# Kernel optimization log

Measured on AMD Instinct MI355X. Metric: run time of the kernel, lower is better.

The kernel has to match this reference:

```python
import jax, jax.numpy as jnp
from jax import lax
import numpy as np

IN_C, OUT_C, K, N_SPLIT = 256, 256, 3, 4
N_LEGO = int(OUT_C * 0.25)          # 64
BASIC_C = IN_C // N_SPLIT           # 64


def setup_inputs() -> dict:
    key = jax.random.key(0)
    k1, k2, k3, k4 = jax.random.split(key, 4)
    x = jax.random.normal(k1, (32, IN_C, 56, 56), dtype=jnp.float32)
    # kaiming-normal-ish initialization of parameters
    lego = jax.random.normal(k2, (N_LEGO, BASIC_C, K, 1), dtype=jnp.float32) * np.sqrt(2.0 / (BASIC_C * K))
    aux_coefficients = jax.random.normal(k3, (N_SPLIT, OUT_C, N_LEGO, 1, 1), dtype=jnp.float32) * np.sqrt(2.0 / N_LEGO)
    aux_combination = jax.random.normal(k4, (N_SPLIT, OUT_C, N_LEGO, 1, 1), dtype=jnp.float32) * np.sqrt(2.0 / N_LEGO)
    return {"x": x, "lego": lego, "aux_coefficients": aux_coefficients, "aux_combination": aux_combination}


def reference(x, lego, aux_coefficients, aux_combination):
    n_split, out_c, n_lego = aux_combination.shape[:3]
    bc = lego.shape[1]
    # one-hot selection: each (split, out_channel) picks exactly one lego feature
    idx = jnp.argmax(aux_combination[..., 0, 0], axis=2)              # (n_split, out_c)
    proxy = jax.nn.one_hot(idx, n_lego, dtype=x.dtype)                # (n_split, out_c, n_lego)
    W = aux_coefficients[..., 0, 0] * proxy                           # (n_split, out_c, n_lego)
    out = 0.0
    for i in range(n_split):
        xi = x[:, i * bc:(i + 1) * bc]                                # (B, bc, H, W)
        feat = lax.conv_general_dilated(
            xi, lego, window_strides=(3, 1), padding=((1, 1), (1, 1)),
            dimension_numbers=("NCHW", "OIHW", "NCHW"))               # (B, n_lego, Ho, Wo)
        out = out + jnp.einsum("bnhw,on->bohw", feat, W[i])
    return out
```

## Files before the change

kernel.cpp:

```cpp
#include <hip/hip_runtime.h>

#define INC    256
#define HIN    56
#define WIN    56
#define HOUT   19
#define WOUT   58
#define KTOT   768

typedef short frag8 __attribute__((ext_vector_type(8)));
typedef float f32x4 __attribute__((ext_vector_type(4)));

static __device__ __forceinline__ unsigned short f2bf(float f) {
    unsigned u = __float_as_uint(f);
    u += 0x7fffu + ((u >> 16) & 1u);
    return (unsigned short)(u >> 16);
}

__global__ __launch_bounds__(256) void prep_weff(
    const float* __restrict__ lego,
    const float* __restrict__ coefs,
    const float* __restrict__ comb,
    unsigned short* __restrict__ Asw)
{
    __shared__ int   idxS[4];
    __shared__ float cofS[4];
    const int t  = threadIdx.x;
    const int kx = blockIdx.x;
    const int o  = blockIdx.y;
    const int wv = t >> 6, l = t & 63;

    float v  = comb[(wv * 256 + o) * 64 + l];
    int   bi = l;
    #pragma unroll
    for (int off = 32; off >= 1; off >>= 1) {
        float ov = __shfl_xor(v, off, 64);
        int   oi = __shfl_xor(bi, off, 64);
        if (ov > v || (ov == v && oi < bi)) { v = ov; bi = oi; }
    }
    if (l == 0) {
        idxS[wv] = bi;
        cofS[wv] = coefs[(wv * 256 + o) * 64 + bi];
    }
    __syncthreads();

    const int k  = kx * 256 + t;
    const int kh = k >> 8, c = k & 255;
    const int i  = c >> 6, cl = c & 63;
    float w = cofS[i] * lego[idxS[i] * 192 + cl * 3 + kh];

    const int o_tile = o >> 4, m = o & 15;
    const int ks = k >> 5, kc = (k >> 3) & 3, j = k & 7;
    Asw[((((size_t)o_tile * 24 + ks) * 64) + kc * 16 + m) * 8 + j] = f2bf(w);
}

__global__ __launch_bounds__(256, 5) void conv_mfma(
    const float* __restrict__ x,
    const unsigned short* __restrict__ Asw,
    float* __restrict__ out)
{
    __shared__ unsigned short Xs[12 * 2 * 64 * 8];

    const int t  = threadIdx.x;
    const int wh = blockIdx.x;
    const int h  = blockIdx.y;
    const int b  = blockIdx.z;

    const int l  = t & 63;
    const int lo = l & 15;
    const int hi = l >> 4;
    const int wv = t >> 6;

    f32x4 acc[4][2];
    #pragma unroll
    for (int ot = 0; ot < 4; ++ot)
        #pragma unroll
        for (int nt = 0; nt < 2; ++nt)
            acc[ot][nt] = (f32x4){0.f, 0.f, 0.f, 0.f};

    const float* xb = x + (size_t)b * (INC * HIN * WIN);
    const int w     = t & 31;
    const int kg    = t >> 5;
    const int col   = wh * 32 - 1 + w;
    const bool colok = (unsigned)col < (unsigned)WIN;
    const int wtile = w >> 4;
    const int lbase = w & 15;
    const int rowbase = 3 * h - 1;

    const frag8* Af = (const frag8*)Asw + ((size_t)(wv * 4) * 24) * 64 + l;
    const frag8* Xf = (const frag8*)Xs + l;

    for (int c2 = 0; c2 < 2; ++c2) {
        #pragma unroll
        for (int q = 0; q < 6; ++q) {
            int p   = kg * 6 + q;
            int ksl = p >> 2, kc = p & 3;
            int kgl = c2 * 384 + ksl * 32 + kc * 8;
            int kh  = kgl >> 8, c0 = kgl & 255;
            int row = rowbase + kh;
            bool ok = colok && ((unsigned)row < (unsigned)HIN);
            const float* xp = xb + (size_t)c0 * (HIN * WIN) + row * WIN + col;
            union { frag8 f; unsigned short u[8]; } pk;
            #pragma unroll
            for (int j = 0; j < 8; ++j) {
                float v = ok ? xp[(size_t)j * (HIN * WIN)] : 0.f;
                pk.u[j] = f2bf(v);
            }
            *(frag8*)&Xs[(((ksl * 2 + wtile) * 64) + kc * 16 + lbase) * 8] = pk.f;
        }
        __syncthreads();

        const int ksb = c2 * 12;
        frag8 a[4], an[4], b0, b1, b0n, b1n;
        #pragma unroll
        for (int ot = 0; ot < 4; ++ot) a[ot] = Af[(ot * 24 + ksb) * 64];
        b0 = Xf[0];
        b1 = Xf[64];

        #pragma unroll
        for (int ks = 0; ks < 11; ++ks) {
            #pragma unroll
            for (int ot = 0; ot < 4; ++ot) an[ot] = Af[(ot * 24 + ksb + ks + 1) * 64];
            b0n = Xf[((ks + 1) * 2) * 64];
            b1n = Xf[((ks + 1) * 2 + 1) * 64];

            #pragma unroll
            for (int ot = 0; ot < 4; ++ot) {
                acc[ot][0] = __builtin_amdgcn_mfma_f32_16x16x32_bf16(a[ot], b0, acc[ot][0], 0, 0, 0);
                acc[ot][1] = __builtin_amdgcn_mfma_f32_16x16x32_bf16(a[ot], b1, acc[ot][1], 0, 0, 0);
            }
            #pragma unroll
            for (int ot = 0; ot < 4; ++ot) a[ot] = an[ot];
            b0 = b0n; b1 = b1n;
        }
        #pragma unroll
        for (int ot = 0; ot < 4; ++ot) {
            acc[ot][0] = __builtin_amdgcn_mfma_f32_16x16x32_bf16(a[ot], b0, acc[ot][0], 0, 0, 0);
            acc[ot][1] = __builtin_amdgcn_mfma_f32_16x16x32_bf16(a[ot], b1, acc[ot][1], 0, 0, 0);
        }
        __syncthreads();
    }

    const int wb = wh * 32;
    const int obase = wv * 64;
    #pragma unroll
    for (int ot = 0; ot < 4; ++ot) {
        #pragma unroll
        for (int nt = 0; nt < 2; ++nt) {
            int wcol = wb + nt * 16 + lo;
            if (wcol < WOUT) {
                #pragma unroll
                for (int r = 0; r < 4; ++r) {
                    int o = obase + ot * 16 + hi * 4 + r;
                    out[((size_t)(b * 256 + o) * HOUT + h) * WOUT + wcol] = acc[ot][nt][r];
                }
            }
        }
    }
}

extern "C" void kernel_launch(void* const* d_in, const int* in_sizes, int n_in,
                              void* d_out, int out_size, void* d_ws, size_t ws_size,
                              hipStream_t stream) {
    const float* x     = (const float*)d_in[0];
    const float* lego  = (const float*)d_in[1];
    const float* coefs = (const float*)d_in[2];
    const float* comb  = (const float*)d_in[3];
    float* out = (float*)d_out;

    unsigned short* Asw = (unsigned short*)d_ws;

    prep_weff<<<dim3(3, 256), 256, 0, stream>>>(lego, coefs, comb, Asw);
    conv_mfma<<<dim3(2, HOUT, 32), 256, 0, stream>>>(x, Asw, out);
}
```

Measured before the change: 194.2 us.

## Prefetch second K-half of input into registers during first-half MFMA loop

Unrolls the two-chunk K loop so that global loads for the second half of the input tile are issued into 48 registers before the first half's MFMA loop runs. After the first compute phase those values are converted to bf16 and stored to shared memory. The goal is to hide global load latency behind MFMA work. The 48 extra live floats raise register pressure and may reduce occupancy under the launch_bounds(256,5) target.

```diff
diff --git a/kernel.cpp b/kernel.cpp
--- a/kernel.cpp
+++ b/kernel.cpp
@@ -70,13 +70,6 @@
     const int hi = l >> 4;
     const int wv = t >> 6;
 
-    f32x4 acc[4][2];
-    #pragma unroll
-    for (int ot = 0; ot < 4; ++ot)
-        #pragma unroll
-        for (int nt = 0; nt < 2; ++nt)
-            acc[ot][nt] = (f32x4){0.f, 0.f, 0.f, 0.f};
-
     const float* xb = x + (size_t)b * (INC * HIN * WIN);
     const int w     = t & 31;
     const int kg    = t >> 5;
@@ -89,55 +82,105 @@
     const frag8* Af = (const frag8*)Asw + ((size_t)(wv * 4) * 24) * 64 + l;
     const frag8* Xf = (const frag8*)Xs + l;
 
-    for (int c2 = 0; c2 < 2; ++c2) {
-        #pragma unroll
-        for (int q = 0; q < 6; ++q) {
-            int p   = kg * 6 + q;
-            int ksl = p >> 2, kc = p & 3;
-            int kgl = c2 * 384 + ksl * 32 + kc * 8;
-            int kh  = kgl >> 8, c0 = kgl & 255;
-            int row = rowbase + kh;
-            bool ok = colok && ((unsigned)row < (unsigned)HIN);
-            const float* xp = xb + (size_t)c0 * (HIN * WIN) + row * WIN + col;
-            union { frag8 f; unsigned short u[8]; } pk;
-            #pragma unroll
-            for (int j = 0; j < 8; ++j) {
-                float v = ok ? xp[(size_t)j * (HIN * WIN)] : 0.f;
-                pk.u[j] = f2bf(v);
-            }
-            *(frag8*)&Xs[(((ksl * 2 + wtile) * 64) + kc * 16 + lbase) * 8] = pk.f;
-        }
-        __syncthreads();
-
-        const int ksb = c2 * 12;
-        frag8 a[4], an[4], b0, b1, b0n, b1n;
-        #pragma unroll
-        for (int ot = 0; ot < 4; ++ot) a[ot] = Af[(ot * 24 + ksb) * 64];
-        b0 = Xf[0];
-        b1 = Xf[64];
-
-        #pragma unroll
-        for (int ks = 0; ks < 11; ++ks) {
-            #pragma unroll
-            for (int ot = 0; ot < 4; ++ot) an[ot] = Af[(ot * 24 + ksb + ks + 1) * 64];
-            b0n = Xf[((ks + 1) * 2) * 64];
-            b1n = Xf[((ks + 1) * 2 + 1) * 64];
-
-            #pragma unroll
-            for (int ot = 0; ot < 4; ++ot) {
-                acc[ot][0] = __builtin_amdgcn_mfma_f32_16x16x32_bf16(a[ot], b0, acc[ot][0], 0, 0, 0);
-                acc[ot][1] = __builtin_amdgcn_mfma_f32_16x16x32_bf16(a[ot], b1, acc[ot][1], 0, 0, 0);
-            }
-            #pragma unroll
-            for (int ot = 0; ot < 4; ++ot) a[ot] = an[ot];
-            b0 = b0n; b1 = b1n;
-        }
+    f32x4 acc[4][2];
+    #pragma unroll
+    for (int ot = 0; ot < 4; ++ot)
+        #pragma unroll
+        for (int nt = 0; nt < 2; ++nt)
+            acc[ot][nt] = (f32x4){0.f, 0.f, 0.f, 0.f};
+
+    float v[48];
+    bool  okq[6];
+    const float* xpq[6];
+
+    #pragma unroll
+    for (int q = 0; q < 6; ++q) {
+        int p = kg * 6 + q, ksl = p >> 2, kc = p & 3;
+        int kk = ksl * 32 + kc * 8;
+        int kh = kk >> 8, c0 = kk & 255;
+        int row = rowbase + kh;
+        bool ok = colok && ((unsigned)row < (unsigned)HIN);
+        okq[q]  = ok;
+        xpq[q]  = ok ? (xb + (size_t)c0 * (HIN * WIN) + row * WIN + col) : xb;
+    }
+    #pragma unroll
+    for (int q = 0; q < 6; ++q)
+        #pragma unroll
+        for (int j = 0; j < 8; ++j)
+            v[q * 8 + j] = xpq[q][(size_t)j * (HIN * WIN)];
+
+    #pragma unroll
+    for (int q = 0; q < 6; ++q) {
+        int p = kg * 6 + q, ksl = p >> 2, kc = p & 3;
+        union { frag8 f; unsigned short u[8]; } pk;
+        #pragma unroll
+        for (int j = 0; j < 8; ++j)
+            pk.u[j] = f2bf(okq[q] ? v[q * 8 + j] : 0.f);
+        *(frag8*)&Xs[(((ksl * 2 + wtile) * 64) + kc * 16 + lbase) * 8] = pk.f;
+    }
+    __syncthreads();
+
+    #pragma unroll
+    for (int q = 0; q < 6; ++q) {
+        int p = kg * 6 + q, ksl = p >> 2, kc = p & 3;
+        int kk = 384 + ksl * 32 + kc * 8;
+        int kh = kk >> 8, c0 = kk & 255;
+        int row = rowbase + kh;
+        bool ok = colok && ((unsigned)row < (unsigned)HIN);
+        okq[q]  = ok;
+        xpq[q]  = ok ? (xb + (size_t)c0 * (HIN * WIN) + row * WIN + col) : xb;
+    }
+    #pragma unroll
+    for (int q = 0; q < 6; ++q)
+        #pragma unroll
+        for (int j = 0; j < 8; ++j)
+            v[q * 8 + j] = xpq[q][(size_t)j * (HIN * WIN)];
+
+    frag8 a[4], an[4];
+    #pragma unroll
+    for (int ks = 0; ks < 12; ++ks) {
+        #pragma unroll
+        for (int ot = 0; ot < 4; ++ot) a[ot] = Af[(ot * 24 + ks) * 64];
+        frag8 b0 = Xf[(ks * 2) * 64];
+        frag8 b1 = Xf[(ks * 2 + 1) * 64];
         #pragma unroll
         for (int ot = 0; ot < 4; ++ot) {
             acc[ot][0] = __builtin_amdgcn_mfma_f32_16x16x32_bf16(a[ot], b0, acc[ot][0], 0, 0, 0);
             acc[ot][1] = __builtin_amdgcn_mfma_f32_16x16x32_bf16(a[ot], b1, acc[ot][1], 0, 0, 0);
         }
-        __syncthreads();
+    }
+    __syncthreads();
+
+    #pragma unroll
+    for (int q = 0; q < 6; ++q) {
+        int p = kg * 6 + q, ksl = p >> 2, kc = p & 3;
+        union { frag8 f; unsigned short u[8]; } pk;
+        #pragma unroll
+        for (int j = 0; j < 8; ++j)
+            pk.u[j] = f2bf(okq[q] ? v[q * 8 + j] : 0.f);
+        *(frag8*)&Xs[(((ksl * 2 + wtile) * 64) + kc * 16 + lbase) * 8] = pk.f;
+    }
+    __syncthreads();
+
+    #pragma unroll
+    for (int ot = 0; ot < 4; ++ot) a[ot] = Af[(ot * 24 + 12) * 64];
+    #pragma unroll
+    for (int ks = 12; ks < 24; ++ks) {
+        frag8 b0 = Xf[((ks - 12) * 2) * 64];
+        frag8 b1 = Xf[((ks - 12) * 2 + 1) * 64];
+        if (ks < 23) {
+            #pragma unroll
+            for (int ot = 0; ot < 4; ++ot) an[ot] = Af[(ot * 24 + ks + 1) * 64];
+        }
+        #pragma unroll
+        for (int ot = 0; ot < 4; ++ot) {
+            acc[ot][0] = __builtin_amdgcn_mfma_f32_16x16x32_bf16(a[ot], b0, acc[ot][0], 0, 0, 0);
+            acc[ot][1] = __builtin_amdgcn_mfma_f32_16x16x32_bf16(a[ot], b1, acc[ot][1], 0, 0, 0);
+        }
+        if (ks < 23) {
+            #pragma unroll
+            for (int ot = 0; ot < 4; ++ot) a[ot] = an[ot];
+        }
     }
 
     const int wb = wh * 32;
```

After: 210.0 us. 8.2% more time.
